# Kernel optimization log

Hardware: AMD Instinct MI355X
Metric: run time of the kernel (lower is better)

The kernel has to match this reference:

```python
import jax, jax.numpy as jnp
import numpy as np
from jax import lax

B_SZ, C_IN, C_OUT, H_IM, W_IM = 2, 128, 128, 64, 64
N_STATE = 16
DT_RANK = 4  # ceil(128/32)


def _ln_cf(x, w, b, eps=1e-6):
    # channels_first LayerNorm over channel dim
    u = x.mean(1, keepdims=True)
    s = ((x - u) ** 2).mean(1, keepdims=True)
    return w[None, :, None, None] * (x - u) / jnp.sqrt(s + eps) + b[None, :, None, None]


def _bn_train(x, g, b, eps=1e-5):
    # BatchNorm2d in training mode (batch statistics, biased variance)
    m = x.mean((0, 2, 3), keepdims=True)
    v = ((x - m) ** 2).mean((0, 2, 3), keepdims=True)
    return g[None, :, None, None] * (x - m) / jnp.sqrt(v + eps) + b[None, :, None, None]


def _dwconv(x, w, b):
    y = lax.conv_general_dilated(x, w, (1, 1), 'SAME', feature_group_count=x.shape[1],
                                 dimension_numbers=('NCHW', 'OIHW', 'NCHW'))
    return y + b[None, :, None, None]


def _conv1x1(x, w, b):
    return jnp.einsum('oi,bihw->bohw', w, x) + b[None, :, None, None]


def _selective_scan(u, dt, A, Bm, Cm, D, delta_bias):
    # u, dt: [B,Ch,L]; A: [Ch,N]; Bm, Cm: [B,N,L]; D: [Ch]
    dt = jax.nn.softplus(dt + delta_bias[None, :, None])
    xs = (dt.transpose(2, 0, 1), u.transpose(2, 0, 1), Bm.transpose(2, 0, 1), Cm.transpose(2, 0, 1))
    h0 = jnp.zeros(u.shape[:2] + (A.shape[1],), u.dtype)

    def step(h, inp):
        dt_t, u_t, b_t, c_t = inp
        dA = jnp.exp(dt_t[..., None] * A)                        # [B,Ch,N]
        h = h * dA + (dt_t * u_t)[..., None] * b_t[:, None, :]   # [B,Ch,N]
        return h, jnp.einsum('bcn,bn->bc', h, c_t)

    _, ys = lax.scan(step, h0, xs)
    return ys.transpose(1, 2, 0) + u * D[None, :, None]


def _ssm_apply(u, Wx, bx, Wdt, bdt, Alog, D, r):
    # u: [B,Ch,L]. Replicates torch row-major .reshape of [(B L),D] -> [B,D,L].
    Bb, Ch, L = u.shape
    N = Alog.shape[1]
    x_flat = u.transpose(0, 2, 1).reshape(Bb * L, Ch)   # 'b c l -> (b l) c'
    x_dbl = x_flat @ Wx.T + bx
    dt = (x_dbl[:, :r] @ Wdt.T + bdt).reshape(Bb, Wdt.shape[0], L)
    Bm = x_dbl[:, r:r + N].reshape(Bb, N, L)
    Cm = x_dbl[:, r + N:].reshape(Bb, N, L)
    return _selective_scan(u, dt, -jnp.exp(Alog), Bm, Cm, D, bdt)


def _forward(x, ln_in_w, ln_in_b, inproj_w, inproj_b, ln_mamba_w, ln_mamba_b, convm_w, convm_b,
             convr_w, convr_b, ln_cat_w, ln_cat_b, xproj_f_w, xproj_f_b, dtproj_f_w, dtproj_f_b,
             Alog_f, D_f, xproj_b_w, xproj_b_b, dtproj_b_w, dtproj_b_b, Alog_b, D_b,
             xproj_u_w, xproj_u_b, dtproj_u_w, dtproj_u_b, Alog_u, D_u, gate1_w, gate1_b,
             bn_g, bn_b, gate2_w, gate2_b, outproj_w, outproj_b, outln_w, outln_b):
    Bb, C, H, W = x.shape
    L = H * W
    half = C // 2
    x = _ln_cf(x, ln_in_w, ln_in_b)
    xp = _conv1x1(x, inproj_w, inproj_b)
    x_mamba, x_res = xp[:, :C], xp[:, C:]
    x_mamba = _ln_cf(x_mamba, ln_mamba_w, ln_mamba_b)
    x_mamba = jax.nn.silu(_dwconv(x_mamba, convm_w, convm_b))
    x_res = jax.nn.silu(_dwconv(x_res, convr_w, convr_b))
    # forward scan on first half of channels
    xf = x_mamba[:, :half].reshape(Bb, half, L)
    yf = _ssm_apply(xf, xproj_f_w, xproj_f_b, dtproj_f_w, dtproj_f_b, Alog_f, D_f, DT_RANK).reshape(Bb, half, H, W)
    # backward scan on second half (flip H,W, scan, flip back)
    xb = x_mamba[:, half:][:, :, ::-1, ::-1]
    yb = _ssm_apply(xb.reshape(Bb, half, L), xproj_b_w, xproj_b_b, dtproj_b_w, dtproj_b_b,
                    Alog_b, D_b, DT_RANK).reshape(Bb, half, H, W)[:, :, ::-1, ::-1]
    concat = _ln_cf(jnp.concatenate([yf, yb], axis=1), ln_cat_w, ln_cat_b)
    # uncertainty-ordered scan on full x_mamba
    sig = jax.nn.sigmoid(x_mamba.mean(1, keepdims=True))
    unc = (-(sig * jnp.log(sig + 1e-6))).reshape(Bb, L)
    idx = jnp.argsort(-unc, axis=1)       # descending uncertainty
    inv = jnp.argsort(idx, axis=1)        # inverse permutation
    xs = jnp.take_along_axis(x_mamba.reshape(Bb, C, L), idx[:, None, :], axis=2)
    yu = _ssm_apply(xs, xproj_u_w, xproj_u_b, dtproj_u_w, dtproj_u_b, Alog_u, D_u, 2 * DT_RANK)
    yu = jnp.take_along_axis(yu, inv[:, None, :], axis=2).reshape(Bb, C, H, W)
    # gated fusion
    g = jax.nn.relu(_bn_train(_conv1x1(jnp.concatenate([concat, yu], 1), gate1_w, gate1_b), bn_g, bn_b))
    g = jax.nn.sigmoid(_conv1x1(g, gate2_w, gate2_b))
    fused = g * yu + (1.0 - g) * concat
    out = _conv1x1(jnp.concatenate([fused, x_res], 1), outproj_w, outproj_b)
    return _ln_cf(out, outln_w, outln_b)


def setup_inputs() -> dict:
    key = jax.random.key(0)
    ks = jax.random.split(key, 16)
    C, half, R, N = C_IN, C_IN // 2, DT_RANK, N_STATE
    rn = lambda k, shp, s=0.02: jax.random.normal(k, shp, jnp.float32) * s

    def inv_dt(k, n):
        dt = jnp.exp(jax.random.uniform(k, (n,)) * (np.log(0.1) - np.log(0.001)) + np.log(0.001))
        dt = jnp.maximum(dt, 1e-4)
        return dt + jnp.log(-jnp.expm1(-dt))

    std = R ** -0.5
    Alog_h = jnp.log(jnp.broadcast_to(jnp.arange(1, N + 1, dtype=jnp.float32), (half, N)))
    Alog_fl = jnp.log(jnp.broadcast_to(jnp.arange(1, N + 1, dtype=jnp.float32), (C, N)))
    return {
        'x': jax.random.normal(ks[0], (B_SZ, C, H_IM, W_IM), jnp.float32),
        'ln_in_w': jnp.ones(C), 'ln_in_b': jnp.zeros(C),
        'inproj_w': rn(ks[1], (2 * C, C)), 'inproj_b': jnp.zeros(2 * C),
        'ln_mamba_w': jnp.ones(C), 'ln_mamba_b': jnp.zeros(C),
        'convm_w': rn(ks[2], (C, 1, 3, 3), 0.1), 'convm_b': jnp.zeros(C),
        'convr_w': rn(ks[3], (C, 1, 3, 3), 0.1), 'convr_b': jnp.zeros(C),
        'ln_cat_w': jnp.ones(C), 'ln_cat_b': jnp.zeros(C),
        'xproj_f_w': rn(ks[4], (R + 2 * N, half)), 'xproj_f_b': jnp.zeros(R + 2 * N),
        'dtproj_f_w': jax.random.uniform(ks[5], (half, R), minval=-std, maxval=std),
        'dtproj_f_b': inv_dt(ks[6], half),
        'Alog_f': Alog_h, 'D_f': jnp.ones(half),
        'xproj_b_w': rn(ks[7], (R + 2 * N, half)), 'xproj_b_b': jnp.zeros(R + 2 * N),
        'dtproj_b_w': jax.random.uniform(ks[8], (half, R), minval=-std, maxval=std),
        'dtproj_b_b': inv_dt(ks[9], half),
        'Alog_b': Alog_h, 'D_b': jnp.ones(half),
        'xproj_u_w': rn(ks[10], (2 * R + 2 * N, C)), 'xproj_u_b': jnp.zeros(2 * R + 2 * N),
        'dtproj_u_w': jax.random.uniform(ks[11], (C, 2 * R), minval=-std, maxval=std),
        'dtproj_u_b': inv_dt(ks[12], C),
        'Alog_u': Alog_fl, 'D_u': jnp.ones(C),
        'gate1_w': rn(ks[13], (C, 2 * C)), 'gate1_b': jnp.zeros(C),
        'bn_g': jnp.ones(C), 'bn_b': jnp.zeros(C),
        'gate2_w': rn(ks[14], (C, C)), 'gate2_b': jnp.zeros(C),
        'outproj_w': rn(ks[15], (C_OUT, 2 * C)), 'outproj_b': jnp.zeros(C_OUT),
        'outln_w': jnp.ones(C_OUT), 'outln_b': jnp.zeros(C_OUT),
    }


def reference(x, ln_in_w, ln_in_b, inproj_w, inproj_b, ln_mamba_w, ln_mamba_b, convm_w, convm_b,
              convr_w, convr_b, ln_cat_w, ln_cat_b, xproj_f_w, xproj_f_b, dtproj_f_w, dtproj_f_b,
              Alog_f, D_f, xproj_b_w, xproj_b_b, dtproj_b_w, dtproj_b_b, Alog_b, D_b,
              xproj_u_w, xproj_u_b, dtproj_u_w, dtproj_u_b, Alog_u, D_u, gate1_w, gate1_b,
              bn_g, bn_b, gate2_w, gate2_b, outproj_w, outproj_b, outln_w, outln_b):
    return _forward(x, ln_in_w, ln_in_b, inproj_w, inproj_b, ln_mamba_w, ln_mamba_b, convm_w, convm_b,
                    convr_w, convr_b, ln_cat_w, ln_cat_b, xproj_f_w, xproj_f_b, dtproj_f_w, dtproj_f_b,
                    Alog_f, D_f, xproj_b_w, xproj_b_b, dtproj_b_w, dtproj_b_b, Alog_b, D_b,
                    xproj_u_w, xproj_u_b, dtproj_u_w, dtproj_u_b, Alog_u, D_u, gate1_w, gate1_b,
                    bn_g, bn_b, gate2_w, gate2_b, outproj_w, outproj_b, outln_w, outln_b)
```

## Files before the change

### kernel.cpp

```cpp
#include <hip/hip_runtime.h>
#include <cstdint>
#include <cstddef>

#define TPB 256

namespace {

constexpr int B_SZ = 2;
constexpr int C    = 128;
constexpr int HALF = 64;
constexpr int L    = 4096;
constexpr int N    = 16;
constexpr int HH   = 64;
constexpr int WW   = 64;
constexpr int ROW  = 48;

__device__ __forceinline__ float softplusf(float x) {
  return fmaxf(x, 0.f) + __logf(1.f + __expf(-fabsf(x)));
}
__device__ __forceinline__ float sigm(float x) { return 1.f / (1.f + __expf(-x)); }

__device__ __forceinline__ unsigned long long unc_key(float u, int i) {
  unsigned m = __float_as_uint(u);
  m = (m & 0x80000000u) ? ~m : (m | 0x80000000u);
  return ((unsigned long long)(~m) << 32) | (unsigned)i;
}

__global__ void k_conv_ln(const float* __restrict__ X, int bsX,
                          const float* __restrict__ lnw, const float* __restrict__ lnb,
                          const float* __restrict__ W, const float* __restrict__ bias,
                          float* __restrict__ Y, int I, int O,
                          float* __restrict__ st1s, float* __restrict__ st1q) {
  constexpr int O_PB = 16;
  __shared__ float Wl[O_PB * 128];
  __shared__ float aw[128], ab[128];
  const int o0 = blockIdx.y * O_PB;
  const int b  = blockIdx.z;
  for (int t = threadIdx.x; t < O_PB * I; t += TPB) {
    int i = t / O_PB, k = t % O_PB;
    Wl[t] = W[(size_t)(o0 + k) * I + i];
  }
  for (int t = threadIdx.x; t < I; t += TPB) { aw[t] = lnw[t]; ab[t] = lnb[t]; }
  __syncthreads();
  const int l = blockIdx.x * TPB + threadIdx.x;
  const float* X0 = X + (size_t)b * bsX + l;
  float s = 0.f, q = 0.f;
#pragma unroll 8
  for (int i = 0; i < I; ++i) {
    float v = X0[(size_t)i * L];
    s += v; q += v * v;
  }
  const float m = s / I;
  const float r = rsqrtf(q / I - m * m + 1e-6f);
  float acc[O_PB];
#pragma unroll
  for (int k = 0; k < O_PB; ++k) acc[k] = bias[o0 + k];
#pragma unroll 4
  for (int i = 0; i < I; ++i) {
    float xv = (X0[(size_t)i * L] - m) * r * aw[i] + ab[i];
#pragma unroll
    for (int k = 0; k < O_PB; ++k) acc[k] += Wl[i * O_PB + k] * xv;
  }
#pragma unroll
  for (int k = 0; k < O_PB; ++k)
    Y[((size_t)b * O + o0 + k) * L + l] = acc[k];
  if (o0 < 128) {
    float ss = 0.f, qq = 0.f;
#pragma unroll
    for (int k = 0; k < O_PB; ++k) { ss += acc[k]; qq += acc[k] * acc[k]; }
    atomicAdd(&st1s[b * L + l], ss);
    atomicAdd(&st1q[b * L + l], qq);
  }
}

__global__ void k_dwconv_t(const float* __restrict__ xp,
                           const float* __restrict__ st1s, const float* __restrict__ st1q,
                           const float* __restrict__ lnw, const float* __restrict__ lnb,
                           const float* __restrict__ Wm, const float* __restrict__ bm,
                           const float* __restrict__ Wr, const float* __restrict__ br,
                           float* __restrict__ xm, float* __restrict__ xr) {
  const int c = blockIdx.y;
  const int z = blockIdx.z;
  const int b = z & 1, mode = z >> 1;
  const int h0 = blockIdx.x * 4;
  __shared__ float T[6][66];
  const float* Xc = xp + ((size_t)b * 2 * C + (mode ? C + c : c)) * L;
  const float lw = mode ? 0.f : lnw[c];
  const float lb2 = mode ? 0.f : lnb[c];
  for (int t = threadIdx.x; t < 6 * 66; t += TPB) {
    int r = t / 66, cc = t % 66 - 1;
    int hh = h0 - 1 + r;
    float v = 0.f;
    if (hh >= 0 && hh < HH && cc >= 0 && cc < WW) {
      int li = hh * WW + cc;
      v = Xc[li];
      if (mode == 0) {
        float sv = st1s[b * L + li], qv = st1q[b * L + li];
        float m = sv * (1.f / 128.f);
        float rr = rsqrtf(qv * (1.f / 128.f) - m * m + 1e-6f);
        v = (v - m) * rr * lw + lb2;
      }
    }
    T[r][t % 66] = v;
  }
  __syncthreads();
  const int hl = threadIdx.x >> 6, w = threadIdx.x & 63;
  const float* W9 = (mode ? Wr : Wm) + c * 9;
  float acc = mode ? br[c] : bm[c];
#pragma unroll
  for (int kh = 0; kh < 3; ++kh)
#pragma unroll
    for (int kw = 0; kw < 3; ++kw)
      acc += T[hl + kh][w + kw] * W9[kh * 3 + kw];
  const int l = (h0 + hl) * WW + w;
  float* Yp = mode ? xr : xm;
  Yp[((size_t)b * C + c) * L + l] = acc * sigm(acc);
}

__global__ void k_unc(const float* __restrict__ xm, float* __restrict__ unc) {
  const int lp = threadIdx.x & 63;
  const int wv = threadIdx.x >> 6;
  const int p  = blockIdx.x * 64 + lp;
  const int b = p / L, l = p % L;
  const float* Xp = xm + (size_t)b * C * L + l;
  float s = 0.f;
#pragma unroll 8
  for (int i = 0; i < 32; ++i) s += Xp[(size_t)(wv * 32 + i) * L];
  __shared__ float r1[4][64];
  r1[wv][lp] = s;
  __syncthreads();
  if (wv == 0) {
    float st = r1[0][lp] + r1[1][lp] + r1[2][lp] + r1[3][lp];
    float sg = sigm(st / C);
    unc[p] = -(sg * __logf(sg + 1e-6f));
  }
}

__global__ void k_rank(const float* __restrict__ unc, int* __restrict__ rankbuf) {
  constexpr int JC = 512;
  __shared__ unsigned long long K[JC];
  const int b  = blockIdx.z;
  const int j0 = blockIdx.y * JC;
  const int i  = blockIdx.x * TPB + threadIdx.x;
  for (int t = threadIdx.x; t < JC; t += TPB)
    K[t] = unc_key(unc[b * L + j0 + t], j0 + t);
  __syncthreads();
  const unsigned long long my = unc_key(unc[b * L + i], i);
  int cnt = 0;
#pragma unroll 8
  for (int j = 0; j < JC; ++j) cnt += (K[j] < my) ? 1 : 0;
  atomicAdd(&rankbuf[b * L + i], cnt);
}

__global__ void k_scatgath(const float* __restrict__ xm, const int* __restrict__ rankbuf,
                           float* __restrict__ xs, int* __restrict__ idx) {
  int t = blockIdx.x * TPB + threadIdx.x;
  int l = t % L, c = (t / L) % C, b = t / (C * L);
  int r = rankbuf[b * L + l];
  xs[((size_t)b * C + c) * L + r] = xm[t];
  if (c == 0) idx[b * L + r] = l;
}

__global__ void k_convx_all(const float* __restrict__ xm, const float* __restrict__ xs,
                            const float* __restrict__ Wf, const float* __restrict__ bf,
                            const float* __restrict__ Wb, const float* __restrict__ bb,
                            const float* __restrict__ Wu, const float* __restrict__ bu,
                            float* __restrict__ XDF, float* __restrict__ XDU) {
  const int z = blockIdx.z;
  const bool isU = z >= 4;
  const int I = isU ? 128 : 64;
  const int O = isU ? 40 : 36;
  const int RT = isU ? 8 : 4;
  const int o0 = blockIdx.y * 4;
  if (o0 >= O) return;
  int b, dir;
  const float *W, *bi;
  if (!isU) { dir = z >> 1; b = z & 1; W = dir ? Wb : Wf; bi = dir ? bb : bf; }
  else      { dir = 0; b = z - 4; W = Wu; bi = bu; }
  __shared__ float Wl[4 * 128];
  for (int t = threadIdx.x; t < 4 * I; t += TPB) {
    int i = t / 4, k = t % 4;
    Wl[t] = W[(size_t)(o0 + k) * I + i];
  }
  __syncthreads();
  const int l = blockIdx.x * TPB + threadIdx.x;
  const int ls = isU ? l : (dir ? (L - 1 - l) : l);
  const float* Xb = isU ? (xs + (size_t)b * C * L)
                        : (xm + ((size_t)b * C + dir * HALF) * L);
  float acc[4];
#pragma unroll
  for (int k = 0; k < 4; ++k) acc[k] = bi[o0 + k];
#pragma unroll 4
  for (int i = 0; i < I; ++i) {
    float xv = Xb[(size_t)i * L + ls];
#pragma unroll
    for (int k = 0; k < 4; ++k) acc[k] += Wl[i * 4 + k] * xv;
  }
  const int slot0 = (o0 < RT) ? o0 : o0 + (16 - RT);
  float* yp = isU ? (XDU + ((size_t)b * L + l) * ROW + slot0)
                  : (XDF + ((size_t)z * L + l) * ROW + slot0);
#pragma unroll
  for (int k = 0; k < 4; ++k) yp[k] = acc[k];
}

__global__ __launch_bounds__(1024) void
k_scan_all(const float* __restrict__ xdblF, const float* __restrict__ xdblU,
           const float* __restrict__ dtf_w, const float* __restrict__ dtf_b,
           const float* __restrict__ dtb_w, const float* __restrict__ dtb_b,
           const float* __restrict__ dtu_w, const float* __restrict__ dtu_b,
           const float* __restrict__ xm, const float* __restrict__ xs,
           const int* __restrict__ idx,
           const float* __restrict__ Alog_f, const float* __restrict__ Alog_b,
           const float* __restrict__ Alog_u,
           const float* __restrict__ D_f, const float* __restrict__ D_b,
           const float* __restrict__ D_u,
           float* __restrict__ yf, float* __restrict__ yb, float* __restrict__ yu) {
  const int blk = blockIdx.x;
  const int tid = threadIdx.x;
  const bool isU = blk >= 256;
  int CsT, RT, c, b, dir;
  const float *Wdt, *bdt, *Alog, *Dv, *xdbl, *Ub;
  const int* idxb = nullptr;
  float* Y;
  if (!isU) {
    CsT = 64; RT = 4;
    int zb = blk >> 6; c = blk & 63; dir = zb >> 1; b = zb & 1;
    Wdt = dir ? dtb_w : dtf_w; bdt = dir ? dtb_b : dtf_b;
    Alog = dir ? Alog_b : Alog_f; Dv = dir ? D_b : D_f;
    xdbl = xdblF + (size_t)zb * L * ROW;
    Ub = xm + ((size_t)b * C + dir * HALF + c) * L;
    Y = (dir ? yb : yf) + ((size_t)b * HALF + c) * L;
  } else {
    CsT = 128; RT = 8;
    int blk2 = blk - 256; b = blk2 >> 7; c = blk2 & 127; dir = 0;
    Wdt = dtu_w; bdt = dtu_b; Alog = Alog_u; Dv = D_u;
    xdbl = xdblU + (size_t)b * L * ROW;
    Ub = xs + ((size_t)b * C + c) * L;
    idxb = idx + b * L;
    Y = yu + ((size_t)b * C + c) * L;
  }
  __shared__ float sW[1024];
  __shared__ float sb2[128];
  __shared__ float4 dtL4[64 * 17];
  __shared__ float4 uL4[64 * 17];
  __shared__ float sA[N][65], sH[N][65];
  for (int t = tid; t < CsT * RT; t += 1024) {
    int csrc = t / RT, r = t % RT;
    sW[r * CsT + csrc] = Wdt[t];
  }
  for (int t = tid; t < CsT; t += 1024) sb2[t] = bdt[t];
  __syncthreads();
  {
    const int chunk_d = tid >> 4;
    const int sq4 = tid & 15;
    const int sq = sq4 * 4;
    const int lsrc = isU ? (c * 32 + (chunk_d >> 1)) : (c * 64 + chunk_d);
    const float* xrp = xdbl + (size_t)lsrc * ROW;
    float xr[8];
    for (int r = 0; r < RT; ++r) xr[r] = xrp[r];
    const float bcc = sb2[c];
    float dv[4], uv[4];
#pragma unroll
    for (int j = 0; j < 4; ++j) {
      int s = sq + j;
      int csrc = isU ? (((chunk_d & 1) << 6) + s) : s;
      float acc = sb2[csrc] + bcc;
      for (int r = 0; r < RT; ++r) acc += sW[r * CsT + csrc] * xr[r];
      int l = (chunk_d << 6) + s;
      dv[j] = softplusf(acc);
      uv[j] = Ub[isU ? l : (dir ? (L - 1 - l) : l)];
    }
    dtL4[chunk_d * 17 + sq4] = make_float4(dv[0], dv[1], dv[2], dv[3]);
    uL4[chunk_d * 17 + sq4]  = make_float4(uv[0], uv[1], uv[2], uv[3]);
  }
  __syncthreads();
  const int n = tid & 15;
  const int chunk = tid >> 4;
  const float a = -__expf(Alog[c * N + n]);
  const float* bp = xdbl + ((size_t)(chunk << 6)) * ROW + 16 + n;
  const float* cp = bp + 16;
  float ap = 1.f, h = 0.f;
#pragma unroll 4
  for (int m = 0; m < 16; ++m) {
    float4 d4 = dtL4[chunk * 17 + m];
    float4 u4 = uL4[chunk * 17 + m];
    float dv[4] = {d4.x, d4.y, d4.z, d4.w};
    float uv[4] = {u4.x, u4.y, u4.z, u4.w};
#pragma unroll
    for (int jj = 0; jj < 4; ++jj) {
      int s = (m << 2) + jj;
      float bn = bp[(size_t)s * ROW];
      float dA = __expf(dv[jj] * a);
      ap *= dA;
      h = h * dA + dv[jj] * uv[jj] * bn;
    }
  }
  sA[n][chunk] = ap; sH[n][chunk] = h;
  __syncthreads();
  {
    const int w = tid >> 6;
    const int k = tid & 63;
    float A = sA[w][k];
    float Bv = sH[w][k];
#pragma unroll
    for (int j = 1; j < 64; j <<= 1) {
      float pa = __shfl_up(A, j);
      float pb = __shfl_up(Bv, j);
      if (k >= j) { Bv = pb * A + Bv; A = pa * A; }
    }
    float hprev = __shfl_up(Bv, 1);
    sH[w][k] = (k == 0) ? 0.f : hprev;
  }
  __syncthreads();
  h = sH[n][chunk];
  const float Dc = Dv[c];
  const float* uLrow = (const float*)&uL4[chunk * 17];
  const bool h1 = (n & 1) != 0, h2 = (n & 2) != 0, h3 = (n & 4) != 0, h4 = (n & 8) != 0;
  float ybuf[4];
#pragma unroll
  for (int q = 0; q < 4; ++q) {
    float v[16];
#pragma unroll
    for (int m = 0; m < 4; ++m) {
      float4 d4 = dtL4[chunk * 17 + (q << 2) + m];
      float4 u4 = uL4[chunk * 17 + (q << 2) + m];
      float dv[4] = {d4.x, d4.y, d4.z, d4.w};
      float uv[4] = {u4.x, u4.y, u4.z, u4.w};
#pragma unroll
      for (int jj = 0; jj < 4; ++jj) {
        int s = (q << 4) + (m << 2) + jj;
        float bn = bp[(size_t)s * ROW];
        float cn = cp[(size_t)s * ROW];
        float dA = __expf(dv[jj] * a);
        h = h * dA + dv[jj] * uv[jj] * bn;
        v[(m << 2) + jj] = h * cn;
      }
    }
    float u8[8];
#pragma unroll
    for (int k2 = 0; k2 < 8; ++k2) {
      float snd = h1 ? v[2 * k2] : v[2 * k2 + 1];
      float t = __shfl_xor(snd, 1);
      u8[k2] = (h1 ? v[2 * k2 + 1] : v[2 * k2]) + t;
    }
    float u4a[4];
#pragma unroll
    for (int k2 = 0; k2 < 4; ++k2) {
      float snd = h2 ? u8[2 * k2] : u8[2 * k2 + 1];
      float t = __shfl_xor(snd, 2);
      u4a[k2] = (h2 ? u8[2 * k2 + 1] : u8[2 * k2]) + t;
    }
    float u2a[2];
#pragma unroll
    for (int k2 = 0; k2 < 2; ++k2) {
      float snd = h3 ? u4a[2 * k2] : u4a[2 * k2 + 1];
      float t = __shfl_xor(snd, 4);
      u2a[k2] = (h3 ? u4a[2 * k2 + 1] : u4a[2 * k2]) + t;
    }
    float snd = h4 ? u2a[0] : u2a[1];
    float t = __shfl_xor(snd, 8);
    float ysum = (h4 ? u2a[1] : u2a[0]) + t;
    float myu = uLrow[(q << 4) + n];
    ybuf[q] = ysum + myu * Dc;
  }
  if (!isU) {
    float* Yp = Y + (chunk << 6);
#pragma unroll
    for (int q = 0; q < 4; ++q) Yp[16 * q + n] = ybuf[q];
  } else {
    const int s0 = chunk << 6;
#pragma unroll
    for (int q = 0; q < 4; ++q) Y[idxb[s0 + 16 * q + n]] = ybuf[q];
  }
}

template <int O_PB>
__global__ void k_gate1(const float* __restrict__ yf, const float* __restrict__ yb,
                        const float* __restrict__ lncw, const float* __restrict__ lncb,
                        const float* __restrict__ yu,
                        const float* __restrict__ W, const float* __restrict__ bias,
                        float* __restrict__ g1,
                        float* __restrict__ st2m, float* __restrict__ st2r,
                        float* __restrict__ bnsum) {
  __shared__ float Wl[O_PB * 256];
  __shared__ float cw[128], cb2[128];
  __shared__ float part[2][O_PB][4];
  const int o0 = blockIdx.y * O_PB;
  const int b  = blockIdx.z;
  for (int t = threadIdx.x; t < O_PB * 256; t += TPB) {
    int i = t / O_PB, k = t % O_PB;
    Wl[t] = W[(size_t)(o0 + k) * 256 + i];
  }
  for (int t = threadIdx.x; t < 128; t += TPB) { cw[t] = lncw[t]; cb2[t] = lncb[t]; }
  __syncthreads();
  const int l = blockIdx.x * TPB + threadIdx.x;
  const float* f0 = yf + (size_t)b * HALF * L + l;
  const float* b0 = yb + (size_t)b * HALF * L + (L - 1 - l);
  const float* u0 = yu + (size_t)b * C * L + l;
  float s = 0.f, s2 = 0.f;
#pragma unroll 8
  for (int i = 0; i < 64; ++i) { float v = f0[(size_t)i * L]; s += v; s2 += v * v; }
#pragma unroll 8
  for (int i = 0; i < 64; ++i) { float v = b0[(size_t)i * L]; s += v; s2 += v * v; }
  const float m = s / C;
  const float r = rsqrtf(s2 / C - m * m + 1e-6f);
  if (blockIdx.y == 0) { st2m[b * L + l] = m; st2r[b * L + l] = r; }
  float acc[O_PB];
#pragma unroll
  for (int k = 0; k < O_PB; ++k) acc[k] = bias[o0 + k];
#pragma unroll 4
  for (int i = 0; i < 64; ++i) {
    float cv = (f0[(size_t)i * L] - m) * r * cw[i] + cb2[i];
#pragma unroll
    for (int k = 0; k < O_PB; ++k) acc[k] += Wl[i * O_PB + k] * cv;
  }
#pragma unroll 4
  for (int i = 0; i < 64; ++i) {
    float cv = (b0[(size_t)i * L] - m) * r * cw[64 + i] + cb2[64 + i];
#pragma unroll
    for (int k = 0; k < O_PB; ++k) acc[k] += Wl[(64 + i) * O_PB + k] * cv;
  }
#pragma unroll 4
  for (int i = 0; i < 128; ++i) {
    float xv = u0[(size_t)i * L];
#pragma unroll
    for (int k = 0; k < O_PB; ++k) acc[k] += Wl[(128 + i) * O_PB + k] * xv;
  }
#pragma unroll
  for (int k = 0; k < O_PB; ++k)
    g1[((size_t)b * C + o0 + k) * L + l] = acc[k];
  const int wv = threadIdx.x >> 6, lnn = threadIdx.x & 63;
#pragma unroll
  for (int k = 0; k < O_PB; ++k) {
    float v = acc[k];
    v += __shfl_xor(v, 1);  v += __shfl_xor(v, 2);  v += __shfl_xor(v, 4);
    v += __shfl_xor(v, 8);  v += __shfl_xor(v, 16); v += __shfl_xor(v, 32);
    if (lnn == 0) part[0][k][wv] = v;
    float q = acc[k] * acc[k];
    q += __shfl_xor(q, 1);  q += __shfl_xor(q, 2);  q += __shfl_xor(q, 4);
    q += __shfl_xor(q, 8);  q += __shfl_xor(q, 16); q += __shfl_xor(q, 32);
    if (lnn == 0) part[1][k][wv] = q;
  }
  __syncthreads();
  if (threadIdx.x < 2 * O_PB) {
    int which = threadIdx.x >= O_PB, k = threadIdx.x % O_PB;
    float v = part[which][k][0] + part[which][k][1] + part[which][k][2] + part[which][k][3];
    atomicAdd(&bnsum[which * 128 + o0 + k], v);
  }
}

template <int O_PB>
__global__ void k_gate2_fuse(const float* __restrict__ g1,
                             const float* __restrict__ bnsum,
                             const float* __restrict__ bn_g, const float* __restrict__ bn_b,
                             const float* __restrict__ W, const float* __restrict__ bias,
                             const float* __restrict__ yu,
                             const float* __restrict__ yf, const float* __restrict__ yb,
                             const float* __restrict__ mean2, const float* __restrict__ rinv2,
                             const float* __restrict__ lncw, const float* __restrict__ lncb,
                             float* __restrict__ fused) {
  __shared__ float Wl[O_PB * 128];
  __shared__ float sc[128], sh[128];
  __shared__ float cwo[O_PB], cbo[O_PB];
  const int o0 = blockIdx.y * O_PB;
  const int b  = blockIdx.z;
  for (int t = threadIdx.x; t < O_PB * 128; t += TPB) {
    int i = t / O_PB, k = t % O_PB;
    Wl[t] = W[(size_t)(o0 + k) * 128 + i];
  }
  for (int t = threadIdx.x; t < 128; t += TPB) {
    float sv = bnsum[t], qv = bnsum[128 + t];
    float mean = sv / (B_SZ * L);
    float var  = qv / (B_SZ * L) - mean * mean;
    float scv = bn_g[t] * rsqrtf(var + 1e-5f);
    sc[t] = scv;
    sh[t] = bn_b[t] - mean * scv;
  }
  if (threadIdx.x < O_PB) {
    cwo[threadIdx.x] = lncw[o0 + threadIdx.x];
    cbo[threadIdx.x] = lncb[o0 + threadIdx.x];
  }
  __syncthreads();
  const int l = blockIdx.x * TPB + threadIdx.x;
  const float m = mean2[b * L + l], r = rinv2[b * L + l];
  const float* Xb = g1 + (size_t)b * C * L + l;
  float acc[O_PB];
#pragma unroll
  for (int k = 0; k < O_PB; ++k) acc[k] = bias[o0 + k];
#pragma unroll 4
  for (int i = 0; i < 128; ++i) {
    float v = fmaxf(Xb[(size_t)i * L] * sc[i] + sh[i], 0.f);
#pragma unroll
    for (int k = 0; k < O_PB; ++k) acc[k] += Wl[i * O_PB + k] * v;
  }
#pragma unroll
  for (int k = 0; k < O_PB; ++k) {
    int o = o0 + k;
    float g = sigm(acc[k]);
    float yuv = yu[((size_t)b * C + o) * L + l];
    float yv = (o < 64) ? yf[((size_t)b * HALF + o) * L + l]
                        : yb[((size_t)b * HALF + (o - 64)) * L + (L - 1 - l)];
    float cv = (yv - m) * r * cwo[k] + cbo[k];
    fused[((size_t)b * C + o) * L + l] = g * yuv + (1.f - g) * cv;
  }
}

template <int O_PB>
__global__ void k_conv1x1_cat2(const float* __restrict__ X1, const float* __restrict__ X2,
                               const float* __restrict__ W, const float* __restrict__ bias,
                               float* __restrict__ Y, int O) {
  __shared__ float Wl[O_PB * 256];
  const int o0 = blockIdx.y * O_PB;
  const int b  = blockIdx.z;
  for (int t = threadIdx.x; t < O_PB * 256; t += TPB) {
    int i = t / O_PB, k = t % O_PB;
    Wl[t] = W[(size_t)(o0 + k) * 256 + i];
  }
  __syncthreads();
  const int l = blockIdx.x * TPB + threadIdx.x;
  const float* Xb1 = X1 + (size_t)b * C * L + l;
  const float* Xb2 = X2 + (size_t)b * C * L + l;
  float acc[O_PB];
#pragma unroll
  for (int k = 0; k < O_PB; ++k) acc[k] = bias[o0 + k];
#pragma unroll 4
  for (int i = 0; i < 128; ++i) {
    float xv = Xb1[(size_t)i * L];
#pragma unroll
    for (int k = 0; k < O_PB; ++k) acc[k] += Wl[i * O_PB + k] * xv;
  }
#pragma unroll 4
  for (int i = 0; i < 128; ++i) {
    float xv = Xb2[(size_t)i * L];
#pragma unroll
    for (int k = 0; k < O_PB; ++k) acc[k] += Wl[(128 + i) * O_PB + k] * xv;
  }
#pragma unroll
  for (int k = 0; k < O_PB; ++k)
    Y[((size_t)b * O + o0 + k) * L + l] = acc[k];
}

__global__ void k_ln_cf(const float* __restrict__ X,
                        const float* __restrict__ w, const float* __restrict__ bchan,
                        float* __restrict__ Y) {
  const int lp = threadIdx.x & 63;
  const int wv = threadIdx.x >> 6;
  const int p  = blockIdx.x * 64 + lp;
  const int b = p / L, l = p % L;
  const float* Xp = X + (size_t)b * C * L + l;
  float s = 0.f, s2 = 0.f;
#pragma unroll 8
  for (int i = 0; i < 32; ++i) {
    float v = Xp[(size_t)(wv * 32 + i) * L];
    s += v; s2 += v * v;
  }
  __shared__ float r1[4][64], r2[4][64];
  r1[wv][lp] = s; r2[wv][lp] = s2;
  __syncthreads();
  float st  = r1[0][lp] + r1[1][lp] + r1[2][lp] + r1[3][lp];
  float s2t = r2[0][lp] + r2[1][lp] + r2[2][lp] + r2[3][lp];
  float mean = st / C;
  float rinv = rsqrtf(s2t / C - mean * mean + 1e-6f);
  float* Yp = Y + (size_t)b * C * L + l;
#pragma unroll 8
  for (int i = 0; i < 32; ++i) {
    int c = wv * 32 + i;
    float v = Xp[(size_t)c * L];
    Yp[(size_t)c * L] = w[c] * (v - mean) * rinv + bchan[c];
  }
}

}

extern "C" void kernel_launch(void* const* d_in, const int* in_sizes, int n_in,
                              void* d_out, int out_size, void* d_ws, size_t ws_size,
                              hipStream_t stream) {
  const float* x         = (const float*)d_in[0];
  const float* ln_in_w   = (const float*)d_in[1];
  const float* ln_in_b   = (const float*)d_in[2];
  const float* inproj_w  = (const float*)d_in[3];
  const float* inproj_b  = (const float*)d_in[4];
  const float* ln_m_w    = (const float*)d_in[5];
  const float* ln_m_b    = (const float*)d_in[6];
  const float* convm_w   = (const float*)d_in[7];
  const float* convm_b   = (const float*)d_in[8];
  const float* convr_w   = (const float*)d_in[9];
  const float* convr_b   = (const float*)d_in[10];
  const float* ln_cat_w  = (const float*)d_in[11];
  const float* ln_cat_b  = (const float*)d_in[12];
  const float* xpf_w     = (const float*)d_in[13];
  const float* xpf_b     = (const float*)d_in[14];
  const float* dtf_w     = (const float*)d_in[15];
  const float* dtf_b     = (const float*)d_in[16];
  const float* Alog_f    = (const float*)d_in[17];
  const float* D_f       = (const float*)d_in[18];
  const float* xpb_w     = (const float*)d_in[19];
  const float* xpb_b     = (const float*)d_in[20];
  const float* dtb_w     = (const float*)d_in[21];
  const float* dtb_b     = (const float*)d_in[22];
  const float* Alog_b    = (const float*)d_in[23];
  const float* D_b       = (const float*)d_in[24];
  const float* xpu_w     = (const float*)d_in[25];
  const float* xpu_b     = (const float*)d_in[26];
  const float* dtu_w     = (const float*)d_in[27];
  const float* dtu_b     = (const float*)d_in[28];
  const float* Alog_u    = (const float*)d_in[29];
  const float* D_u       = (const float*)d_in[30];
  const float* gate1_w   = (const float*)d_in[31];
  const float* gate1_b   = (const float*)d_in[32];
  const float* bn_g      = (const float*)d_in[33];
  const float* bn_b      = (const float*)d_in[34];
  const float* gate2_w   = (const float*)d_in[35];
  const float* gate2_b   = (const float*)d_in[36];
  const float* outproj_w = (const float*)d_in[37];
  const float* outproj_b = (const float*)d_in[38];
  const float* outln_w   = (const float*)d_in[39];
  const float* outln_b   = (const float*)d_in[40];

  float* ws = (float*)d_ws;
  size_t off = 0;
  auto alloc = [&](size_t n) { float* p = ws + off; off += n; return p; };

  const size_t BL = (size_t)B_SZ * L;
  float* st1s  = alloc(BL);
  float* st1q  = alloc(BL);
  int*   rank  = (int*)alloc(BL);
  float* bnsum = alloc(256);
  const size_t zeroBytes = (3 * BL + 256) * sizeof(float);

  float* xp    = alloc((size_t)B_SZ * 2 * C * L);
  float* xm    = alloc((size_t)B_SZ * C * L);
  float* xr    = alloc((size_t)B_SZ * C * L);
  float* unc   = alloc(BL);
  int*   idx   = (int*)alloc(BL);
  float* xs    = alloc((size_t)B_SZ * C * L);
  float* xdblF = alloc((size_t)4 * L * ROW);
  float* xdblU = alloc((size_t)2 * L * ROW);
  float* yf    = alloc((size_t)B_SZ * HALF * L);
  float* yb    = alloc((size_t)B_SZ * HALF * L);
  float* yu    = alloc((size_t)B_SZ * C * L);
  float* st2m  = alloc(BL);
  float* st2r  = alloc(BL);
  float* g1    = alloc((size_t)B_SZ * C * L);
  float* fused = alloc((size_t)B_SZ * C * L);
  float* outp  = alloc((size_t)B_SZ * C * L);
  (void)ws_size; (void)in_sizes; (void)n_in; (void)out_size;

  const int pixB = B_SZ * L / 64;
  const int elemB = B_SZ * C * L / TPB;

  hipMemsetAsync(st1s, 0, zeroBytes, stream);
  k_conv_ln<<<dim3(L / TPB, 16, B_SZ), TPB, 0, stream>>>(
      x, C * L, ln_in_w, ln_in_b, inproj_w, inproj_b, xp, 128, 256, st1s, st1q);
  k_dwconv_t<<<dim3(HH / 4, C, 2 * B_SZ), TPB, 0, stream>>>(
      xp, st1s, st1q, ln_m_w, ln_m_b, convm_w, convm_b, convr_w, convr_b, xm, xr);
  k_unc<<<pixB, TPB, 0, stream>>>(xm, unc);
  k_rank<<<dim3(L / TPB, 8, B_SZ), TPB, 0, stream>>>(unc, rank);
  k_scatgath<<<elemB, TPB, 0, stream>>>(xm, rank, xs, idx);
  k_convx_all<<<dim3(L / TPB, 10, 6), TPB, 0, stream>>>(
      xm, xs, xpf_w, xpf_b, xpb_w, xpb_b, xpu_w, xpu_b, xdblF, xdblU);
  k_scan_all<<<512, 1024, 0, stream>>>(
      xdblF, xdblU, dtf_w, dtf_b, dtb_w, dtb_b, dtu_w, dtu_b,
      xm, xs, idx, Alog_f, Alog_b, Alog_u, D_f, D_b, D_u, yf, yb, yu);
  k_gate1<16><<<dim3(L / TPB, 8, B_SZ), TPB, 0, stream>>>(
      yf, yb, ln_cat_w, ln_cat_b, yu, gate1_w, gate1_b, g1, st2m, st2r, bnsum);
  k_gate2_fuse<16><<<dim3(L / TPB, 8, B_SZ), TPB, 0, stream>>>(
      g1, bnsum, bn_g, bn_b, gate2_w, gate2_b, yu, yf, yb, st2m, st2r,
      ln_cat_w, ln_cat_b, fused);
  k_conv1x1_cat2<16><<<dim3(L / TPB, 8, B_SZ), TPB, 0, stream>>>(
      fused, xr, outproj_w, outproj_b, outp, 128);
  k_ln_cf<<<pixB, TPB, 0, stream>>>(outp, outln_w, outln_b, (float*)d_out);
}
```

Measured before the change: 346.0 us.

## Split LayerNorms out of 1x1 convs, halve output-channel tiles, fuse out-LN stats

Moves the input LayerNorm and the concat LayerNorm into separate per-pixel kernels that write normalized tensors, so the 1x1-conv kernels no longer recompute statistics and normalization in every output-channel block. Output channels per block drop from 16 to 8, doubling grid size for occupancy, and unroll factors rise to 8. The output projection accumulates per-pixel sum and sum-of-squares via atomics, so the final LayerNorm becomes a vectorized elementwise pass. This costs extra full-tensor writes and reads (xln, ycat) and more atomics, and each input is re-read by twice as many blocks.

```diff
diff --git a/kernel.cpp b/kernel.cpp
--- a/kernel.cpp
+++ b/kernel.cpp
@@ -26,44 +26,95 @@
   return ((unsigned long long)(~m) << 32) | (unsigned)i;
 }
 
-__global__ void k_conv_ln(const float* __restrict__ X, int bsX,
-                          const float* __restrict__ lnw, const float* __restrict__ lnb,
+__global__ void k_pixln(const float* __restrict__ X, const float* __restrict__ w,
+                        const float* __restrict__ bchan, float* __restrict__ Y) {
+  const int px = threadIdx.x & 31;
+  const int g  = threadIdx.x >> 5;
+  const int p  = blockIdx.x * 32 + px;
+  const int b  = p / L, l = p % L;
+  const float* Xp = X + (size_t)b * C * L + l;
+  float v[16];
+  float s = 0.f, s2 = 0.f;
+#pragma unroll
+  for (int j = 0; j < 16; ++j) {
+    float t = Xp[(size_t)(g * 16 + j) * L];
+    v[j] = t; s += t; s2 += t * t;
+  }
+  __shared__ float red[2][8][32];
+  red[0][g][px] = s; red[1][g][px] = s2;
+  __syncthreads();
+  float st = 0.f, qt = 0.f;
+#pragma unroll
+  for (int k = 0; k < 8; ++k) { st += red[0][k][px]; qt += red[1][k][px]; }
+  const float m = st * (1.f / C);
+  const float r = rsqrtf(qt * (1.f / C) - m * m + 1e-6f);
+  float* Yp = Y + (size_t)b * C * L + l;
+#pragma unroll
+  for (int j = 0; j < 16; ++j) {
+    int c = g * 16 + j;
+    Yp[(size_t)c * L] = w[c] * (v[j] - m) * r + bchan[c];
+  }
+}
+
+__global__ void k_lncat(const float* __restrict__ yf, const float* __restrict__ yb,
+                        const float* __restrict__ w, const float* __restrict__ bchan,
+                        float* __restrict__ Y) {
+  const int px = threadIdx.x & 31;
+  const int g  = threadIdx.x >> 5;
+  const int p  = blockIdx.x * 32 + px;
+  const int b  = p / L, l = p % L;
+  float v[16];
+  float s = 0.f, s2 = 0.f;
+#pragma unroll
+  for (int j = 0; j < 16; ++j) {
+    int c = g * 16 + j;
+    float t = (c < 64) ? yf[((size_t)b * HALF + c) * L + l]
+                       : yb[((size_t)b * HALF + (c - 64)) * L + (L - 1 - l)];
+    v[j] = t; s += t; s2 += t * t;
+  }
+  __shared__ float red[2][8][32];
+  red[0][g][px] = s; red[1][g][px] = s2;
+  __syncthreads();
+  float st = 0.f, qt = 0.f;
+#pragma unroll
+  for (int k = 0; k < 8; ++k) { st += red[0][k][px]; qt += red[1][k][px]; }
+  const float m = st * (1.f / C);
+  const float r = rsqrtf(qt * (1.f / C) - m * m + 1e-6f);
+  float* Yp = Y + (size_t)b * C * L + l;
+#pragma unroll
+  for (int j = 0; j < 16; ++j) {
+    int c = g * 16 + j;
+    Yp[(size_t)c * L] = w[c] * (v[j] - m) * r + bchan[c];
+  }
+}
+
+__global__ void k_conv_in(const float* __restrict__ X,
                           const float* __restrict__ W, const float* __restrict__ bias,
-                          float* __restrict__ Y, int I, int O,
+                          float* __restrict__ Y,
                           float* __restrict__ st1s, float* __restrict__ st1q) {
-  constexpr int O_PB = 16;
+  constexpr int O_PB = 8;
   __shared__ float Wl[O_PB * 128];
-  __shared__ float aw[128], ab[128];
   const int o0 = blockIdx.y * O_PB;
   const int b  = blockIdx.z;
-  for (int t = threadIdx.x; t < O_PB * I; t += TPB) {
+  for (int t = threadIdx.x; t < O_PB * 128; t += TPB) {
     int i = t / O_PB, k = t % O_PB;
-    Wl[t] = W[(size_t)(o0 + k) * I + i];
-  }
-  for (int t = threadIdx.x; t < I; t += TPB) { aw[t] = lnw[t]; ab[t] = lnb[t]; }
+    Wl[t] = W[(size_t)(o0 + k) * 128 + i];
+  }
   __syncthreads();
   const int l = blockIdx.x * TPB + threadIdx.x;
-  const float* X0 = X + (size_t)b * bsX + l;
-  float s = 0.f, q = 0.f;
-#pragma unroll 8
-  for (int i = 0; i < I; ++i) {
-    float v = X0[(size_t)i * L];
-    s += v; q += v * v;
-  }
-  const float m = s / I;
-  const float r = rsqrtf(q / I - m * m + 1e-6f);
+  const float* X0 = X + (size_t)b * C * L + l;
   float acc[O_PB];
 #pragma unroll
   for (int k = 0; k < O_PB; ++k) acc[k] = bias[o0 + k];
-#pragma unroll 4
-  for (int i = 0; i < I; ++i) {
-    float xv = (X0[(size_t)i * L] - m) * r * aw[i] + ab[i];
+#pragma unroll 8
+  for (int i = 0; i < 128; ++i) {
+    float xv = X0[(size_t)i * L];
 #pragma unroll
     for (int k = 0; k < O_PB; ++k) acc[k] += Wl[i * O_PB + k] * xv;
   }
 #pragma unroll
   for (int k = 0; k < O_PB; ++k)
-    Y[((size_t)b * O + o0 + k) * L + l] = acc[k];
+    Y[((size_t)b * 256 + o0 + k) * L + l] = acc[k];
   if (o0 < 128) {
     float ss = 0.f, qq = 0.f;
 #pragma unroll
@@ -190,7 +241,7 @@
   float acc[4];
 #pragma unroll
   for (int k = 0; k < 4; ++k) acc[k] = bi[o0 + k];
-#pragma unroll 4
+#pragma unroll 8
   for (int i = 0; i < I; ++i) {
     float xv = Xb[(size_t)i * L + ls];
 #pragma unroll
@@ -375,15 +426,10 @@
 }
 
 template <int O_PB>
-__global__ void k_gate1(const float* __restrict__ yf, const float* __restrict__ yb,
-                        const float* __restrict__ lncw, const float* __restrict__ lncb,
-                        const float* __restrict__ yu,
+__global__ void k_gate1(const float* __restrict__ ycat, const float* __restrict__ yu,
                         const float* __restrict__ W, const float* __restrict__ bias,
-                        float* __restrict__ g1,
-                        float* __restrict__ st2m, float* __restrict__ st2r,
-                        float* __restrict__ bnsum) {
+                        float* __restrict__ g1, float* __restrict__ bnsum) {
   __shared__ float Wl[O_PB * 256];
-  __shared__ float cw[128], cb2[128];
   __shared__ float part[2][O_PB][4];
   const int o0 = blockIdx.y * O_PB;
   const int b  = blockIdx.z;
@@ -391,36 +437,20 @@
     int i = t / O_PB, k = t % O_PB;
     Wl[t] = W[(size_t)(o0 + k) * 256 + i];
   }
-  for (int t = threadIdx.x; t < 128; t += TPB) { cw[t] = lncw[t]; cb2[t] = lncb[t]; }
   __syncthreads();
   const int l = blockIdx.x * TPB + threadIdx.x;
-  const float* f0 = yf + (size_t)b * HALF * L + l;
-  const float* b0 = yb + (size_t)b * HALF * L + (L - 1 - l);
+  const float* c0 = ycat + (size_t)b * C * L + l;
   const float* u0 = yu + (size_t)b * C * L + l;
-  float s = 0.f, s2 = 0.f;
-#pragma unroll 8
-  for (int i = 0; i < 64; ++i) { float v = f0[(size_t)i * L]; s += v; s2 += v * v; }
-#pragma unroll 8
-  for (int i = 0; i < 64; ++i) { float v = b0[(size_t)i * L]; s += v; s2 += v * v; }
-  const float m = s / C;
-  const float r = rsqrtf(s2 / C - m * m + 1e-6f);
-  if (blockIdx.y == 0) { st2m[b * L + l] = m; st2r[b * L + l] = r; }
   float acc[O_PB];
 #pragma unroll
   for (int k = 0; k < O_PB; ++k) acc[k] = bias[o0 + k];
-#pragma unroll 4
-  for (int i = 0; i < 64; ++i) {
-    float cv = (f0[(size_t)i * L] - m) * r * cw[i] + cb2[i];
+#pragma unroll 8
+  for (int i = 0; i < 128; ++i) {
+    float cv = c0[(size_t)i * L];
 #pragma unroll
     for (int k = 0; k < O_PB; ++k) acc[k] += Wl[i * O_PB + k] * cv;
   }
-#pragma unroll 4
-  for (int i = 0; i < 64; ++i) {
-    float cv = (b0[(size_t)i * L] - m) * r * cw[64 + i] + cb2[64 + i];
-#pragma unroll
-    for (int k = 0; k < O_PB; ++k) acc[k] += Wl[(64 + i) * O_PB + k] * cv;
-  }
-#pragma unroll 4
+#pragma unroll 8
   for (int i = 0; i < 128; ++i) {
     float xv = u0[(size_t)i * L];
 #pragma unroll
@@ -454,14 +484,10 @@
                              const float* __restrict__ bnsum,
                              const float* __restrict__ bn_g, const float* __restrict__ bn_b,
                              const float* __restrict__ W, const float* __restrict__ bias,
-                             const float* __restrict__ yu,
-                             const float* __restrict__ yf, const float* __restrict__ yb,
-                             const float* __restrict__ mean2, const float* __restrict__ rinv2,
-                             const float* __restrict__ lncw, const float* __restrict__ lncb,
+                             const float* __restrict__ yu, const float* __restrict__ ycat,
                              float* __restrict__ fused) {
   __shared__ float Wl[O_PB * 128];
   __shared__ float sc[128], sh[128];
-  __shared__ float cwo[O_PB], cbo[O_PB];
   const int o0 = blockIdx.y * O_PB;
   const int b  = blockIdx.z;
   for (int t = threadIdx.x; t < O_PB * 128; t += TPB) {
@@ -476,18 +502,13 @@
     sc[t] = scv;
     sh[t] = bn_b[t] - mean * scv;
   }
-  if (threadIdx.x < O_PB) {
-    cwo[threadIdx.x] = lncw[o0 + threadIdx.x];
-    cbo[threadIdx.x] = lncb[o0 + threadIdx.x];
-  }
   __syncthreads();
   const int l = blockIdx.x * TPB + threadIdx.x;
-  const float m = mean2[b * L + l], r = rinv2[b * L + l];
   const float* Xb = g1 + (size_t)b * C * L + l;
   float acc[O_PB];
 #pragma unroll
   for (int k = 0; k < O_PB; ++k) acc[k] = bias[o0 + k];
-#pragma unroll 4
+#pragma unroll 8
   for (int i = 0; i < 128; ++i) {
     float v = fmaxf(Xb[(size_t)i * L] * sc[i] + sh[i], 0.f);
 #pragma unroll
@@ -498,17 +519,16 @@
     int o = o0 + k;
     float g = sigm(acc[k]);
     float yuv = yu[((size_t)b * C + o) * L + l];
-    float yv = (o < 64) ? yf[((size_t)b * HALF + o) * L + l]
-                        : yb[((size_t)b * HALF + (o - 64)) * L + (L - 1 - l)];
-    float cv = (yv - m) * r * cwo[k] + cbo[k];
+    float cv = ycat[((size_t)b * C + o) * L + l];
     fused[((size_t)b * C + o) * L + l] = g * yuv + (1.f - g) * cv;
   }
 }
 
 template <int O_PB>
-__global__ void k_conv1x1_cat2(const float* __restrict__ X1, const float* __restrict__ X2,
-                               const float* __restrict__ W, const float* __restrict__ bias,
-                               float* __restrict__ Y, int O) {
+__global__ void k_outproj(const float* __restrict__ X1, const float* __restrict__ X2,
+                          const float* __restrict__ W, const float* __restrict__ bias,
+                          float* __restrict__ Y,
+                          float* __restrict__ st3s, float* __restrict__ st3q) {
   __shared__ float Wl[O_PB * 256];
   const int o0 = blockIdx.y * O_PB;
   const int b  = blockIdx.z;
@@ -523,51 +543,63 @@
   float acc[O_PB];
 #pragma unroll
   for (int k = 0; k < O_PB; ++k) acc[k] = bias[o0 + k];
-#pragma unroll 4
+#pragma unroll 8
   for (int i = 0; i < 128; ++i) {
     float xv = Xb1[(size_t)i * L];
 #pragma unroll
     for (int k = 0; k < O_PB; ++k) acc[k] += Wl[i * O_PB + k] * xv;
   }
-#pragma unroll 4
+#pragma unroll 8
   for (int i = 0; i < 128; ++i) {
     float xv = Xb2[(size_t)i * L];
 #pragma unroll
     for (int k = 0; k < O_PB; ++k) acc[k] += Wl[(128 + i) * O_PB + k] * xv;
   }
-#pragma unroll
-  for (int k = 0; k < O_PB; ++k)
-    Y[((size_t)b * O + o0 + k) * L + l] = acc[k];
-}
-
-__global__ void k_ln_cf(const float* __restrict__ X,
-                        const float* __restrict__ w, const float* __restrict__ bchan,
-                        float* __restrict__ Y) {
-  const int lp = threadIdx.x & 63;
-  const int wv = threadIdx.x >> 6;
-  const int p  = blockIdx.x * 64 + lp;
-  const int b = p / L, l = p % L;
-  const float* Xp = X + (size_t)b * C * L + l;
-  float s = 0.f, s2 = 0.f;
-#pragma unroll 8
-  for (int i = 0; i < 32; ++i) {
-    float v = Xp[(size_t)(wv * 32 + i) * L];
-    s += v; s2 += v * v;
-  }
-  __shared__ float r1[4][64], r2[4][64];
-  r1[wv][lp] = s; r2[wv][lp] = s2;
-  __syncthreads();
-  float st  = r1[0][lp] + r1[1][lp] + r1[2][lp] + r1[3][lp];
-  float s2t = r2[0][lp] + r2[1][lp] + r2[2][lp] + r2[3][lp];
-  float mean = st / C;
-  float rinv = rsqrtf(s2t / C - mean * mean + 1e-6f);
-  float* Yp = Y + (size_t)b * C * L + l;
-#pragma unroll 8
-  for (int i = 0; i < 32; ++i) {
-    int c = wv * 32 + i;
-    float v = Xp[(size_t)c * L];
-    Yp[(size_t)c * L] = w[c] * (v - mean) * rinv + bchan[c];
-  }
+  float ss = 0.f, qq = 0.f;
+#pragma unroll
+  for (int k = 0; k < O_PB; ++k) {
+    Y[((size_t)b * C + o0 + k) * L + l] = acc[k];
+    ss += acc[k]; qq += acc[k] * acc[k];
+  }
+  atomicAdd(&st3s[b * L + l], ss);
+  atomicAdd(&st3q[b * L + l], qq);
+}
+
+__global__ void k_ln_out(const float* __restrict__ X,
+                         const float* __restrict__ st3s, const float* __restrict__ st3q,
+                         const float* __restrict__ w, const float* __restrict__ bchan,
+                         float* __restrict__ Y) {
+  const int t  = blockIdx.x * TPB + threadIdx.x;
+  const int gi = t * 4;
+  const int l  = gi % L;
+  const int c  = (gi / L) % C;
+  const int b  = gi / (C * L);
+  const float4 v  = ((const float4*)X)[t];
+  const float4 s4 = *(const float4*)(st3s + b * L + l);
+  const float4 q4 = *(const float4*)(st3q + b * L + l);
+  const float wc = w[c], bc = bchan[c];
+  float4 o;
+  {
+    float m = s4.x * (1.f / C);
+    float r = rsqrtf(q4.x * (1.f / C) - m * m + 1e-6f);
+    o.x = wc * (v.x - m) * r + bc;
+  }
+  {
+    float m = s4.y * (1.f / C);
+    float r = rsqrtf(q4.y * (1.f / C) - m * m + 1e-6f);
+    o.y = wc * (v.y - m) * r + bc;
+  }
+  {
+    float m = s4.z * (1.f / C);
+    float r = rsqrtf(q4.z * (1.f / C) - m * m + 1e-6f);
+    o.z = wc * (v.z - m) * r + bc;
+  }
+  {
+    float m = s4.w * (1.f / C);
+    float r = rsqrtf(q4.w * (1.f / C) - m * m + 1e-6f);
+    o.w = wc * (v.w - m) * r + bc;
+  }
+  ((float4*)Y)[t] = o;
 }
 
 }
@@ -624,10 +656,13 @@
   const size_t BL = (size_t)B_SZ * L;
   float* st1s  = alloc(BL);
   float* st1q  = alloc(BL);
+  float* st3s  = alloc(BL);
+  float* st3q  = alloc(BL);
   int*   rank  = (int*)alloc(BL);
   float* bnsum = alloc(256);
-  const size_t zeroBytes = (3 * BL + 256) * sizeof(float);
-
+  const size_t zeroBytes = (5 * BL + 256) * sizeof(float);
+
+  float* xln   = alloc((size_t)B_SZ * C * L);
   float* xp    = alloc((size_t)B_SZ * 2 * C * L);
   float* xm    = alloc((size_t)B_SZ * C * L);
   float* xr    = alloc((size_t)B_SZ * C * L);
@@ -639,19 +674,20 @@
   float* yf    = alloc((size_t)B_SZ * HALF * L);
   float* yb    = alloc((size_t)B_SZ * HALF * L);
   float* yu    = alloc((size_t)B_SZ * C * L);
-  float* st2m  = alloc(BL);
-  float* st2r  = alloc(BL);
+  float* ycat  = alloc((size_t)B_SZ * C * L);
   float* g1    = alloc((size_t)B_SZ * C * L);
   float* fused = alloc((size_t)B_SZ * C * L);
   float* outp  = alloc((size_t)B_SZ * C * L);
   (void)ws_size; (void)in_sizes; (void)n_in; (void)out_size;
 
-  const int pixB = B_SZ * L / 64;
-  const int elemB = B_SZ * C * L / TPB;
+  const int pixB   = B_SZ * L / 64;
+  const int pixB32 = B_SZ * L / 32;
+  const int elemB  = B_SZ * C * L / TPB;
 
   hipMemsetAsync(st1s, 0, zeroBytes, stream);
-  k_conv_ln<<<dim3(L / TPB, 16, B_SZ), TPB, 0, stream>>>(
-      x, C * L, ln_in_w, ln_in_b, inproj_w, inproj_b, xp, 128, 256, st1s, st1q);
+  k_pixln<<<pixB32, TPB, 0, stream>>>(x, ln_in_w, ln_in_b, xln);
+  k_conv_in<<<dim3(L / TPB, 32, B_SZ), TPB, 0, stream>>>(
+      xln, inproj_w, inproj_b, xp, st1s, st1q);
   k_dwconv_t<<<dim3(HH / 4, C, 2 * B_SZ), TPB, 0, stream>>>(
       xp, st1s, st1q, ln_m_w, ln_m_b, convm_w, convm_b, convr_w, convr_b, xm, xr);
   k_unc<<<pixB, TPB, 0, stream>>>(xm, unc);
@@ -662,12 +698,13 @@
   k_scan_all<<<512, 1024, 0, stream>>>(
       xdblF, xdblU, dtf_w, dtf_b, dtb_w, dtb_b, dtu_w, dtu_b,
       xm, xs, idx, Alog_f, Alog_b, Alog_u, D_f, D_b, D_u, yf, yb, yu);
-  k_gate1<16><<<dim3(L / TPB, 8, B_SZ), TPB, 0, stream>>>(
-      yf, yb, ln_cat_w, ln_cat_b, yu, gate1_w, gate1_b, g1, st2m, st2r, bnsum);
-  k_gate2_fuse<16><<<dim3(L / TPB, 8, B_SZ), TPB, 0, stream>>>(
-      g1, bnsum, bn_g, bn_b, gate2_w, gate2_b, yu, yf, yb, st2m, st2r,
-      ln_cat_w, ln_cat_b, fused);
-  k_conv1x1_cat2<16><<<dim3(L / TPB, 8, B_SZ), TPB, 0, stream>>>(
-      fused, xr, outproj_w, outproj_b, outp, 128);
-  k_ln_cf<<<pixB, TPB, 0, stream>>>(outp, outln_w, outln_b, (float*)d_out);
-}
+  k_lncat<<<pixB32, TPB, 0, stream>>>(yf, yb, ln_cat_w, ln_cat_b, ycat);
+  k_gate1<8><<<dim3(L / TPB, 16, B_SZ), TPB, 0, stream>>>(
+      ycat, yu, gate1_w, gate1_b, g1, bnsum);
+  k_gate2_fuse<8><<<dim3(L / TPB, 16, B_SZ), TPB, 0, stream>>>(
+      g1, bnsum, bn_g, bn_b, gate2_w, gate2_b, yu, ycat, fused);
+  k_outproj<8><<<dim3(L / TPB, 16, B_SZ), TPB, 0, stream>>>(
+      fused, xr, outproj_w, outproj_b, outp, st3s, st3q);
+  k_ln_out<<<(B_SZ * C * L / 4) / TPB, TPB, 0, stream>>>(
+      outp, st3s, st3q, outln_w, outln_b, (float*)d_out);
+}
```

Result: faster. 291.7 us (-15.7%).
